# Optimization experiments

Hardware: AMD Instinct MI355X
Metric: run time of the kernel (lower is better)

## Reference

```python
import jax, jax.numpy as jnp
import numpy as np

B, T, D = 2, 2048, 1024
D_LABEL = D // 2
N_LABELS = 50


def setup_inputs() -> dict:
    key = jax.random.key(0)
    ks = jax.random.split(key, 10)
    dep = jax.random.normal(ks[0], (B, T, D), dtype=jnp.float32)
    head = jax.random.normal(ks[1], (B, T + 1, D), dtype=jnp.float32)
    head_indices = jax.random.randint(ks[2], (B, T), 0, T + 1)
    mask = jnp.ones((B, T), dtype=bool)
    # learned params
    lim_p = 1.0 / np.sqrt(D)
    dep_W = jax.random.uniform(ks[3], (D_LABEL, D), minval=-lim_p, maxval=lim_p, dtype=jnp.float32)
    dep_b = jax.random.uniform(ks[4], (D_LABEL,), minval=-lim_p, maxval=lim_p, dtype=jnp.float32)
    head_W = jax.random.uniform(ks[5], (D_LABEL, D), minval=-lim_p, maxval=lim_p, dtype=jnp.float32)
    head_b = jax.random.uniform(ks[6], (D_LABEL,), minval=-lim_p, maxval=lim_p, dtype=jnp.float32)
    # xavier_uniform over last two dims of W
    lim_w = np.sqrt(6.0 / (D_LABEL + D_LABEL))
    W = jax.random.uniform(ks[7], (N_LABELS, D_LABEL, D_LABEL), minval=-lim_w, maxval=lim_w, dtype=jnp.float32)
    bias = jnp.zeros((N_LABELS,), dtype=jnp.float32)
    return {"dep": dep, "head": head, "head_indices": head_indices, "mask": mask,
            "dep_W": dep_W, "dep_b": dep_b, "head_W": head_W, "head_b": head_b,
            "W": W, "bias": bias}


def reference(dep, head, head_indices, mask, dep_W, dep_b, head_W, head_b, W, bias):
    # project to label space [B,T,d_label] / [B,T+1,d_label]
    dep_label = jnp.einsum('btd,ed->bte', dep, dep_W) + dep_b
    head_label = jnp.einsum('btd,ed->bte', head, head_W) + head_b
    # gather predicted head rep per token: [B,T,d_label]
    selected = jnp.take_along_axis(head_label, head_indices[..., None], axis=1)
    # biaffine scoring: dep^T W_n head for each label n -> [B,T,n_labels]
    logits = jnp.einsum('btd,nde,bte->btn', dep_label, W, selected)
    return logits + bias[None, None, :]
```

## Files before the change

kernel.cpp:

```cpp
#include <hip/hip_runtime.h>
#include <hip/hip_bf16.h>
#include <cstdint>

typedef __bf16 bf16;
typedef bf16 bf16x8 __attribute__((ext_vector_type(8)));
typedef float f32x4 __attribute__((ext_vector_type(4)));

#define NTOK 4096
#define DLBL 512
#define NLAB 50

__device__ inline bf16x8 cvt8(float4 a, float4 b) {
  bf16x8 r;
  r[0] = (bf16)a.x; r[1] = (bf16)a.y; r[2] = (bf16)a.z; r[3] = (bf16)a.w;
  r[4] = (bf16)b.x; r[5] = (bf16)b.y; r[6] = (bf16)b.z; r[7] = (bf16)b.w;
  return r;
}

__device__ __forceinline__ void gl16(const bf16* g, void* l) {
  __builtin_amdgcn_global_load_lds(
      (const __attribute__((address_space(1))) void*)g,
      (__attribute__((address_space(3))) void*)l, 16, 0, 0);
}

__device__ void projA_body(int bidx, const float* __restrict__ Wp,
                           const float* __restrict__ X,
                           const float* __restrict__ bv,
                           bf16* __restrict__ outT, char* lds) {
  char* ldsA = lds;
  char* ldsB = lds + 10240;
  const int tid = threadIdx.x, l = tid & 63, w = tid >> 6;
  const int tokbase = (bidx >> 2) * 64;
  const int ebase   = (bidx & 3) * 128;
  const int wr = w & 1, wc = w >> 1;
  f32x4 acc[4][2] = {};
  const int arow = tid >> 1, ahalf = tid & 1;
  const int brow = tid >> 2, bgr = tid & 3;
  const float* aS = Wp + (size_t)(ebase + arow) * 1024 + ahalf * 16;
  const float* bS = X  + (size_t)(tokbase + brow) * 1024 + bgr * 8;
  const int lo = (l & 15) * 80 + (l >> 4) * 16;
  for (int kb = 0; kb < 1024; kb += 32) {
    float4 a0 = *(const float4*)(aS + kb);
    float4 a1 = *(const float4*)(aS + kb + 4);
    float4 a2 = *(const float4*)(aS + kb + 8);
    float4 a3 = *(const float4*)(aS + kb + 12);
    float4 b0 = *(const float4*)(bS + kb);
    float4 b1 = *(const float4*)(bS + kb + 4);
    *(bf16x8*)(ldsA + arow * 80 + ahalf * 32)      = cvt8(a0, a1);
    *(bf16x8*)(ldsA + arow * 80 + ahalf * 32 + 16) = cvt8(a2, a3);
    *(bf16x8*)(ldsB + brow * 80 + bgr * 16)        = cvt8(b0, b1);
    __syncthreads();
    bf16x8 aF[4], bF[2];
#pragma unroll
    for (int i = 0; i < 4; ++i) aF[i] = *(bf16x8*)(ldsA + (wr * 64 + i * 16) * 80 + lo);
#pragma unroll
    for (int j = 0; j < 2; ++j) bF[j] = *(bf16x8*)(ldsB + (wc * 32 + j * 16) * 80 + lo);
#pragma unroll
    for (int i = 0; i < 4; ++i)
#pragma unroll
      for (int j = 0; j < 2; ++j)
        acc[i][j] = __builtin_amdgcn_mfma_f32_16x16x32_bf16(aF[i], bF[j], acc[i][j], 0, 0, 0);
    __syncthreads();
  }
#pragma unroll
  for (int i = 0; i < 4; ++i)
#pragma unroll
    for (int j = 0; j < 2; ++j)
#pragma unroll
      for (int r = 0; r < 4; ++r) {
        int eg = ebase + wr * 64 + i * 16 + (l >> 4) * 4 + r;
        int tg = tokbase + wc * 32 + j * 16 + (l & 15);
        outT[(size_t)eg * NTOK + tg] = (bf16)(acc[i][j][r] + bv[eg]);
      }
}

__device__ void projB_body(int bidx, const float* __restrict__ head,
                           const int* __restrict__ hidx,
                           const float* __restrict__ Wp,
                           const float* __restrict__ bv,
                           bf16* __restrict__ selO, char* lds) {
  char* ldsA = lds;
  char* ldsB = lds + 10240;
  const int tid = threadIdx.x, l = tid & 63, w = tid >> 6;
  const int tokbase = (bidx >> 3) * 128;
  const int ebase   = (bidx & 7) * 64;
  const int wr = w & 1, wc = w >> 1;
  f32x4 acc[4][2] = {};
  const int arow = tid >> 1, ahalf = tid & 1;
  const int brow = tid >> 2, bgr = tid & 3;
  const int flat = tokbase + arow;
  const int bb = flat >> 11;
  const int hv = hidx[flat];
  const float* aS = head + ((size_t)bb * 2049 + hv) * 1024 + ahalf * 16;
  const float* bS = Wp + (size_t)(ebase + brow) * 1024 + bgr * 8;
  const int lo = (l & 15) * 80 + (l >> 4) * 16;
  for (int kb = 0; kb < 1024; kb += 32) {
    float4 a0 = *(const float4*)(aS + kb);
    float4 a1 = *(const float4*)(aS + kb + 4);
    float4 a2 = *(const float4*)(aS + kb + 8);
    float4 a3 = *(const float4*)(aS + kb + 12);
    float4 b0 = *(const float4*)(bS + kb);
    float4 b1 = *(const float4*)(bS + kb + 4);
    *(bf16x8*)(ldsA + arow * 80 + ahalf * 32)      = cvt8(a0, a1);
    *(bf16x8*)(ldsA + arow * 80 + ahalf * 32 + 16) = cvt8(a2, a3);
    *(bf16x8*)(ldsB + brow * 80 + bgr * 16)        = cvt8(b0, b1);
    __syncthreads();
    bf16x8 aF[4], bF[2];
#pragma unroll
    for (int i = 0; i < 4; ++i) aF[i] = *(bf16x8*)(ldsA + (wr * 64 + i * 16) * 80 + lo);
#pragma unroll
    for (int j = 0; j < 2; ++j) bF[j] = *(bf16x8*)(ldsB + (wc * 32 + j * 16) * 80 + lo);
#pragma unroll
    for (int i = 0; i < 4; ++i)
#pragma unroll
      for (int j = 0; j < 2; ++j)
        acc[i][j] = __builtin_amdgcn_mfma_f32_16x16x32_bf16(aF[i], bF[j], acc[i][j], 0, 0, 0);
    __syncthreads();
  }
#pragma unroll
  for (int i = 0; i < 4; ++i)
#pragma unroll
    for (int j = 0; j < 2; ++j)
#pragma unroll
      for (int r = 0; r < 4; ++r) {
        int tg = tokbase + wr * 64 + i * 16 + (l >> 4) * 4 + r;
        int eg = ebase + wc * 32 + j * 16 + (l & 15);
        selO[(size_t)tg * DLBL + eg] = (bf16)(acc[i][j][r] + bv[eg]);
      }
}

__global__ __launch_bounds__(256) void prep_k(const float* __restrict__ W,
                                              bf16* __restrict__ Wb,
                                              const float* __restrict__ dep_W,
                                              const float* __restrict__ dep,
                                              const float* __restrict__ dep_b,
                                              bf16* __restrict__ depT,
                                              const float* __restrict__ head,
                                              const int* __restrict__ hidx,
                                              const float* __restrict__ head_W,
                                              const float* __restrict__ head_b,
                                              bf16* __restrict__ selB) {
  __shared__ char lds[15360];
  const int b = blockIdx.x;
  if (b < 256) {
    projA_body(b, dep_W, dep, dep_b, depT, lds);
  } else if (b < 512) {
    projB_body(b - 256, head, hidx, head_W, head_b, selB, lds);
  } else {
    int i = (b - 512) * 256 + threadIdx.x;
    const float4* s = (const float4*)W + (size_t)i * 2;
    float4 a = s[0], c = s[1];
    *(bf16x8*)(Wb + (size_t)i * 8) = cvt8(a, c);
  }
}

__global__ __launch_bounds__(512, 4) void biaff_k(const bf16* __restrict__ Wb,
                                                  const bf16* __restrict__ sel,
                                                  const bf16* __restrict__ depT,
                                                  float* __restrict__ parts) {
  __shared__ char lds[73728];
  const int tid = threadIdx.x, l = tid & 63, w = tid >> 6;

  const int lin = blockIdx.x;
  const int xcd = lin & 7, idx = lin >> 3;
  const int sub = idx % 25;
  const int bx  = idx / 25;
  const int combo = xcd * 25 + sub;
  const int n  = combo % 50;
  const int dz = combo / 50;
  const int tokbase = bx * 256;
  const int dbase   = dz * 128;

  const int wd = w >> 2, wt = w & 3;
  f32x4 acc[4][4] = {};

  const int srow = l >> 2;
  const int schunk = ((l & 3) ^ ((l >> 3) & 3)) * 8;
  const bf16* aG = Wb  + ((size_t)(n * DLBL + dbase + w * 16 + srow)) * DLBL + schunk;
  const bf16* bG = sel + ((size_t)(tokbase + w * 32 + srow)) * DLBL + schunk;
  const int aOff = w * 1024;
  const int bOff = 8192 + w * 2048;

  const int lq = l & 15, lh = l >> 4;
  const int ro = lh ^ ((lq >> 1) & 3);
  const char* rdA = lds + (wd * 64 + lq) * 64 + ro * 16;
  const char* rdB = lds + 8192 + (wt * 64 + lq) * 64 + ro * 16;

#define STG(T) do { \
    const bf16* a_ = aG + (T) * 32; \
    const bf16* b_ = bG + (T) * 32; \
    char* la_ = lds + ((T) % 3) * 24576 + aOff; \
    char* lb_ = lds + ((T) % 3) * 24576 + bOff; \
    gl16(a_, la_); \
    gl16(b_, lb_); \
    gl16(b_ + 16 * DLBL, lb_ + 1024); \
  } while (0)
#define WAITV(N) asm volatile("s_waitcnt vmcnt(" #N ")" ::: "memory")
#define PHASE(T, DOSTG, DOWV3, DOWV0, DOBAR) do { \
    const char* cA = rdA + ((T) % 3) * 24576; \
    const char* cB = rdB + ((T) % 3) * 24576; \
    bf16x8 aF[4], bF[4]; \
    aF[0] = *(const bf16x8*)(cA + 0 * 1024); \
    aF[1] = *(const bf16x8*)(cA + 1 * 1024); \
    aF[2] = *(const bf16x8*)(cA + 2 * 1024); \
    aF[3] = *(const bf16x8*)(cA + 3 * 1024); \
    bF[0] = *(const bf16x8*)(cB + 0 * 1024); \
    bF[1] = *(const bf16x8*)(cB + 1 * 1024); \
    bF[2] = *(const bf16x8*)(cB + 2 * 1024); \
    bF[3] = *(const bf16x8*)(cB + 3 * 1024); \
    if (DOSTG) STG((T) + 2); \
    __builtin_amdgcn_s_setprio(1); \
    _Pragma("unroll") \
    for (int i = 0; i < 4; ++i) \
      _Pragma("unroll") \
      for (int j = 0; j < 4; ++j) \
        acc[i][j] = __builtin_amdgcn_mfma_f32_16x16x32_bf16(aF[i], bF[j], acc[i][j], 0, 0, 0); \
    __builtin_amdgcn_s_setprio(0); \
    if (DOWV3) WAITV(3); \
    if (DOWV0) WAITV(0); \
    if (DOBAR) __builtin_amdgcn_s_barrier(); \
  } while (0)

  STG(0); STG(1);
  WAITV(3);
  __builtin_amdgcn_s_barrier();

  PHASE(0, 1, 1, 0, 1);  PHASE(1, 1, 1, 0, 1);  PHASE(2, 1, 1, 0, 1);
  PHASE(3, 1, 1, 0, 1);  PHASE(4, 1, 1, 0, 1);  PHASE(5, 1, 1, 0, 1);
  PHASE(6, 1, 1, 0, 1);  PHASE(7, 1, 1, 0, 1);  PHASE(8, 1, 1, 0, 1);
  PHASE(9, 1, 1, 0, 1);  PHASE(10, 1, 1, 0, 1); PHASE(11, 1, 1, 0, 1);
  PHASE(12, 1, 1, 0, 1); PHASE(13, 1, 1, 0, 1);
  PHASE(14, 0, 0, 1, 1);
  PHASE(15, 0, 0, 0, 0);

#undef PHASE
#undef WAITV
#undef STG

  float p[4] = {0.f, 0.f, 0.f, 0.f};
#pragma unroll
  for (int j = 0; j < 4; ++j) {
    const int tg = tokbase + wt * 64 + j * 16 + lq;
#pragma unroll
    for (int i = 0; i < 4; ++i)
#pragma unroll
      for (int r = 0; r < 4; ++r) {
        int dg = dbase + wd * 64 + i * 16 + lh * 4 + r;
        p[j] += acc[i][j][r] * (float)depT[(size_t)dg * NTOK + tg];
      }
  }
#pragma unroll
  for (int j = 0; j < 4; ++j) {
    p[j] += __shfl_xor(p[j], 16);
    p[j] += __shfl_xor(p[j], 32);
  }
  if (l < 16) {
#pragma unroll
    for (int j = 0; j < 4; ++j) {
      int tg = tokbase + wt * 64 + j * 16 + l;
      parts[(size_t)(dz * 2 + wd) * 204800 + (size_t)tg * NLAB + n] = p[j];
    }
  }
}

__global__ __launch_bounds__(256) void fin_k(const float* __restrict__ parts,
                                             const float* __restrict__ bias,
                                             float* __restrict__ out) {
  int i = blockIdx.x * 256 + threadIdx.x;
  float v = 0.f;
#pragma unroll
  for (int q = 0; q < 8; ++q) v += parts[(size_t)q * 204800 + i];
  out[i] = v + bias[i % NLAB];
}

extern "C" void kernel_launch(void* const* d_in, const int* in_sizes, int n_in,
                              void* d_out, int out_size, void* d_ws, size_t ws_size,
                              hipStream_t stream) {
  const float* dep    = (const float*)d_in[0];
  const float* head   = (const float*)d_in[1];
  const int*   hidx   = (const int*)d_in[2];
  const float* dep_W  = (const float*)d_in[4];
  const float* dep_b  = (const float*)d_in[5];
  const float* head_W = (const float*)d_in[6];
  const float* head_b = (const float*)d_in[7];
  const float* W      = (const float*)d_in[8];
  const float* bias   = (const float*)d_in[9];
  float* out = (float*)d_out;

  char* ws = (char*)d_ws;
  bf16*  Wb    = (bf16*)(ws);
  bf16*  depT  = (bf16*)(ws + 26214400);
  bf16*  selB  = (bf16*)(ws + 30408704);
  float* parts = (float*)(ws + 34603008);
  if (ws_size < (size_t)41156608) return;

  hipLaunchKernelGGL(prep_k, dim3(6912), dim3(256), 0, stream,
                     W, Wb, dep_W, dep, dep_b, depT, head, hidx, head_W, head_b, selB);
  hipLaunchKernelGGL(biaff_k, dim3(3200), dim3(512), 0, stream,
                     Wb, selB, depT, parts);
  hipLaunchKernelGGL(fin_k, dim3(800), dim3(256), 0, stream, parts, bias, out);
}
```

Measured before the change: 164.7 us.

## Fuse W fp32-to-bf16 conversion into biaffine kernel's register-staged pipeline

Drops the separate pass that converted the 50x512x512 W tensor to bf16 in prep_k, which wrote and later re-read about 26MB of workspace. biaff_k now loads fp32 W tiles into registers three stages ahead, converts them to bf16 in registers and stores them to LDS. B tiles still use direct global-to-LDS loads. In exchange W is read as fp32 (twice the bytes per tile, possibly re-read across token blocks), and the kernel needs extra registers and lgkmcnt waits before each barrier.

```diff
diff --git a/kernel.cpp b/kernel.cpp
--- a/kernel.cpp
+++ b/kernel.cpp
@@ -129,9 +129,7 @@
       }
 }
 
-__global__ __launch_bounds__(256) void prep_k(const float* __restrict__ W,
-                                              bf16* __restrict__ Wb,
-                                              const float* __restrict__ dep_W,
+__global__ __launch_bounds__(256) void prep_k(const float* __restrict__ dep_W,
                                               const float* __restrict__ dep,
                                               const float* __restrict__ dep_b,
                                               bf16* __restrict__ depT,
@@ -142,19 +140,11 @@
                                               bf16* __restrict__ selB) {
   __shared__ char lds[15360];
   const int b = blockIdx.x;
-  if (b < 256) {
-    projA_body(b, dep_W, dep, dep_b, depT, lds);
-  } else if (b < 512) {
-    projB_body(b - 256, head, hidx, head_W, head_b, selB, lds);
-  } else {
-    int i = (b - 512) * 256 + threadIdx.x;
-    const float4* s = (const float4*)W + (size_t)i * 2;
-    float4 a = s[0], c = s[1];
-    *(bf16x8*)(Wb + (size_t)i * 8) = cvt8(a, c);
-  }
-}
-
-__global__ __launch_bounds__(512, 4) void biaff_k(const bf16* __restrict__ Wb,
+  if (b < 256) projA_body(b, dep_W, dep, dep_b, depT, lds);
+  else         projB_body(b - 256, head, hidx, head_W, head_b, selB, lds);
+}
+
+__global__ __launch_bounds__(512, 4) void biaff_k(const float* __restrict__ Wf,
                                                   const bf16* __restrict__ sel,
                                                   const bf16* __restrict__ depT,
                                                   float* __restrict__ parts) {
@@ -176,9 +166,9 @@
 
   const int srow = l >> 2;
   const int schunk = ((l & 3) ^ ((l >> 3) & 3)) * 8;
-  const bf16* aG = Wb  + ((size_t)(n * DLBL + dbase + w * 16 + srow)) * DLBL + schunk;
-  const bf16* bG = sel + ((size_t)(tokbase + w * 32 + srow)) * DLBL + schunk;
-  const int aOff = w * 1024;
+  const float* aGf = Wf + ((size_t)(n * DLBL + dbase + w * 16 + srow)) * DLBL + schunk;
+  const bf16*  bG  = sel + ((size_t)(tokbase + w * 32 + srow)) * DLBL + schunk;
+  char* wrA = lds + w * 1024 + l * 16;
   const int bOff = 8192 + w * 2048;
 
   const int lq = l & 15, lh = l >> 4;
@@ -186,17 +176,21 @@
   const char* rdA = lds + (wd * 64 + lq) * 64 + ro * 16;
   const char* rdB = lds + 8192 + (wt * 64 + lq) * 64 + ro * 16;
 
-#define STG(T) do { \
-    const bf16* a_ = aG + (T) * 32; \
+  float4 rsa, rsb, rta, rtb;
+
+#define WAITV(N) asm volatile("s_waitcnt vmcnt(" #N ")" ::: "memory")
+#define WAITL    asm volatile("s_waitcnt lgkmcnt(0)" ::: "memory")
+#define STGB(T) do { \
     const bf16* b_ = bG + (T) * 32; \
-    char* la_ = lds + ((T) % 3) * 24576 + aOff; \
     char* lb_ = lds + ((T) % 3) * 24576 + bOff; \
-    gl16(a_, la_); \
     gl16(b_, lb_); \
     gl16(b_ + 16 * DLBL, lb_ + 1024); \
   } while (0)
-#define WAITV(N) asm volatile("s_waitcnt vmcnt(" #N ")" ::: "memory")
-#define PHASE(T, DOSTG, DOWV3, DOWV0, DOBAR) do { \
+#define LDA(T, Ra, Rb) do { \
+    const float4* p_ = (const float4*)(aGf + (T) * 32); \
+    Ra = p_[0]; Rb = p_[1]; \
+  } while (0)
+#define PHASE(T, Ra, Rb, DOCVT, DOB, DOA, DOW4, DOW2, DOW0, DOBAR) do { \
     const char* cA = rdA + ((T) % 3) * 24576; \
     const char* cB = rdB + ((T) % 3) * 24576; \
     bf16x8 aF[4], bF[4]; \
@@ -208,7 +202,9 @@
     bF[1] = *(const bf16x8*)(cB + 1 * 1024); \
     bF[2] = *(const bf16x8*)(cB + 2 * 1024); \
     bF[3] = *(const bf16x8*)(cB + 3 * 1024); \
-    if (DOSTG) STG((T) + 2); \
+    if (DOCVT) *(bf16x8*)(wrA + (((T) + 1) % 3) * 24576) = cvt8(Ra, Rb); \
+    if (DOB) STGB((T) + 2); \
+    if (DOA) LDA((T) + 3, Ra, Rb); \
     __builtin_amdgcn_s_setprio(1); \
     _Pragma("unroll") \
     for (int i = 0; i < 4; ++i) \
@@ -216,26 +212,44 @@
       for (int j = 0; j < 4; ++j) \
         acc[i][j] = __builtin_amdgcn_mfma_f32_16x16x32_bf16(aF[i], bF[j], acc[i][j], 0, 0, 0); \
     __builtin_amdgcn_s_setprio(0); \
-    if (DOWV3) WAITV(3); \
-    if (DOWV0) WAITV(0); \
-    if (DOBAR) __builtin_amdgcn_s_barrier(); \
+    if (DOW4) WAITV(4); \
+    if (DOW2) WAITV(2); \
+    if (DOW0) WAITV(0); \
+    if (DOBAR) { WAITL; __builtin_amdgcn_s_barrier(); } \
   } while (0)
 
-  STG(0); STG(1);
-  WAITV(3);
+  LDA(0, rsa, rsb);
+  WAITV(0);
+  *(bf16x8*)(wrA) = cvt8(rsa, rsb);
+  LDA(2, rsa, rsb);
+  LDA(1, rta, rtb);
+  STGB(0); STGB(1);
+  WAITV(2);
+  WAITL;
   __builtin_amdgcn_s_barrier();
 
-  PHASE(0, 1, 1, 0, 1);  PHASE(1, 1, 1, 0, 1);  PHASE(2, 1, 1, 0, 1);
-  PHASE(3, 1, 1, 0, 1);  PHASE(4, 1, 1, 0, 1);  PHASE(5, 1, 1, 0, 1);
-  PHASE(6, 1, 1, 0, 1);  PHASE(7, 1, 1, 0, 1);  PHASE(8, 1, 1, 0, 1);
-  PHASE(9, 1, 1, 0, 1);  PHASE(10, 1, 1, 0, 1); PHASE(11, 1, 1, 0, 1);
-  PHASE(12, 1, 1, 0, 1); PHASE(13, 1, 1, 0, 1);
-  PHASE(14, 0, 0, 1, 1);
-  PHASE(15, 0, 0, 0, 0);
+  PHASE(0,  rta, rtb, 1, 1, 1, 1, 0, 0, 1);
+  PHASE(1,  rsa, rsb, 1, 1, 1, 1, 0, 0, 1);
+  PHASE(2,  rta, rtb, 1, 1, 1, 1, 0, 0, 1);
+  PHASE(3,  rsa, rsb, 1, 1, 1, 1, 0, 0, 1);
+  PHASE(4,  rta, rtb, 1, 1, 1, 1, 0, 0, 1);
+  PHASE(5,  rsa, rsb, 1, 1, 1, 1, 0, 0, 1);
+  PHASE(6,  rta, rtb, 1, 1, 1, 1, 0, 0, 1);
+  PHASE(7,  rsa, rsb, 1, 1, 1, 1, 0, 0, 1);
+  PHASE(8,  rta, rtb, 1, 1, 1, 1, 0, 0, 1);
+  PHASE(9,  rsa, rsb, 1, 1, 1, 1, 0, 0, 1);
+  PHASE(10, rta, rtb, 1, 1, 1, 1, 0, 0, 1);
+  PHASE(11, rsa, rsb, 1, 1, 1, 1, 0, 0, 1);
+  PHASE(12, rta, rtb, 1, 1, 1, 1, 0, 0, 1);
+  PHASE(13, rsa, rsb, 1, 1, 0, 0, 1, 0, 1);
+  PHASE(14, rta, rtb, 1, 0, 0, 0, 0, 1, 1);
+  PHASE(15, rta, rtb, 0, 0, 0, 0, 0, 0, 0);
 
 #undef PHASE
+#undef LDA
+#undef STGB
+#undef WAITL
 #undef WAITV
-#undef STG
 
   float p[4] = {0.f, 0.f, 0.f, 0.f};
 #pragma unroll
@@ -288,15 +302,14 @@
   float* out = (float*)d_out;
 
   char* ws = (char*)d_ws;
-  bf16*  Wb    = (bf16*)(ws);
-  bf16*  depT  = (bf16*)(ws + 26214400);
-  bf16*  selB  = (bf16*)(ws + 30408704);
-  float* parts = (float*)(ws + 34603008);
-  if (ws_size < (size_t)41156608) return;
-
-  hipLaunchKernelGGL(prep_k, dim3(6912), dim3(256), 0, stream,
-                     W, Wb, dep_W, dep, dep_b, depT, head, hidx, head_W, head_b, selB);
+  bf16*  depT  = (bf16*)(ws);
+  bf16*  selB  = (bf16*)(ws + 4194304);
+  float* parts = (float*)(ws + 8388608);
+  if (ws_size < (size_t)14942208) return;
+
+  hipLaunchKernelGGL(prep_k, dim3(512), dim3(256), 0, stream,
+                     dep_W, dep, dep_b, depT, head, hidx, head_W, head_b, selB);
   hipLaunchKernelGGL(biaff_k, dim3(3200), dim3(512), 0, stream,
-                     Wb, selB, depT, parts);
+                     W, selB, depT, parts);
   hipLaunchKernelGGL(fin_k, dim3(800), dim3(256), 0, stream, parts, bias, out);
 }
```

After: 186.9 us. 1.13x slower.
